# Optimization experiments

Hardware: AMD Instinct MI355X
Metric: run time of the kernel (lower is better)

The kernel has to match this reference:

```python
import jax, jax.numpy as jnp
import numpy as np
from jax import lax

NUM_VARS = 16384
NUM_CHECKS = 8192
BATCH = 32
MAX_ITER = 15
H_DENSITY = 0.001  # ~8 ones per column, LDPC-like Tanner graph


def setup_inputs() -> dict:
    key = jax.random.key(0)
    k_h, k_s, k_l = jax.random.split(key, 3)
    # Sparse binary parity-check matrix represented densely (same math).
    parity_matrix = (jax.random.uniform(k_h, (NUM_CHECKS, NUM_VARS)) < H_DENSITY).astype(jnp.float32)
    syndrome = jax.random.randint(k_s, (BATCH, NUM_CHECKS), 0, 2).astype(jnp.float32)
    channel_llrs = jax.random.normal(k_l, (BATCH, NUM_VARS), dtype=jnp.float32)
    w_vc = jnp.ones((1,), dtype=jnp.float32)
    w_cv = jnp.ones((1,), dtype=jnp.float32)
    damping = jnp.float32(0.5)
    return {
        "syndrome": syndrome,
        "parity_matrix": parity_matrix,
        "channel_llrs": channel_llrs,
        "w_vc": w_vc,
        "w_cv": w_cv,
        "damping": damping,
    }


def reference(syndrome, parity_matrix, channel_llrs, w_vc, w_cv, damping):
    # syndrome: (B, C); parity_matrix H: (C, V); channel_llrs: (B, V)
    s_sign = 1.0 - 2.0 * syndrome  # (B, C)

    def body(v_beliefs, _):
        # v -> c: sparse.mm(H, v^T)^T == v @ H^T  -> (B, C)
        v_to_c = w_vc * (v_beliefs @ parity_matrix.T)
        c_msg = s_sign * jnp.tanh(v_to_c * 0.5)  # (B, C)
        # c -> v: sparse.mm(H^T, c^T)^T == c @ H  -> (B, V)
        c_to_v = w_cv * (c_msg @ parity_matrix)
        v_new = damping * v_beliefs + (1.0 - damping) * (channel_llrs + c_to_v)
        return v_new, None

    v_beliefs, _ = lax.scan(body, channel_llrs, None, length=MAX_ITER)
    return jax.nn.sigmoid(-v_beliefs)  # (B, V) bit-flip probabilities
```

## Files before the change

### kernel.cpp

```cpp
#include <hip/hip_runtime.h>


#define C_NUM 8192
#define V_NUM 16384
#define B_NUM 32
#define RW 64
#define CW 32

__global__ void build_csr(const float* __restrict__ H,
                          int* __restrict__ row_cnt, int* __restrict__ col_cnt,
                          int* __restrict__ row_idx, int* __restrict__ col_idx) {
    const long long total4 = (long long)C_NUM * V_NUM / 4;
    const long long stride = (long long)gridDim.x * blockDim.x;
    for (long long t = (long long)blockIdx.x * blockDim.x + threadIdx.x;
         t < total4; t += stride) {
        float4 hv = ((const float4*)H)[t];
        long long e = t * 4;
        float vals[4] = {hv.x, hv.y, hv.z, hv.w};
#pragma unroll
        for (int k = 0; k < 4; ++k) {
            if (vals[k] != 0.0f) {
                long long ee = e + k;
                int c = (int)(ee >> 14);
                int v = (int)(ee & (V_NUM - 1));
                int rs = atomicAdd(&row_cnt[c], 1);
                if (rs < RW) row_idx[c * RW + rs] = v;
                int cs = atomicAdd(&col_cnt[v], 1);
                if (cs < CW) col_idx[v * CW + cs] = c;
            }
        }
    }
}

__global__ void init_state(const float* __restrict__ llr,
                           const float* __restrict__ synd,
                           float* __restrict__ beliefs, float* __restrict__ llr_t,
                           float* __restrict__ ssign_t) {
    int t = blockIdx.x * blockDim.x + threadIdx.x;
    if (t < V_NUM * B_NUM) {
        int b = t & (B_NUM - 1);
        int v = t >> 5;
        float x = llr[b * V_NUM + v];
        beliefs[t] = x;
        llr_t[t] = x;
    }
    if (t < C_NUM * B_NUM) {
        int b = t & (B_NUM - 1);
        int c = t >> 5;
        ssign_t[t] = 1.0f - 2.0f * synd[b * C_NUM + c];
    }
}

__global__ void vc_kernel(const float* __restrict__ beliefs,
                          const int* __restrict__ row_cnt,
                          const int* __restrict__ row_idx,
                          const float* __restrict__ ssign_t,
                          const float* __restrict__ w_vc_p,
                          float* __restrict__ cmsg) {
    int t = blockIdx.x * blockDim.x + threadIdx.x;
    if (t >= C_NUM * B_NUM) return;
    int b = t & (B_NUM - 1);
    int c = t >> 5;
    float w = w_vc_p[0];
    int n = row_cnt[c];
    if (n > RW) n = RW;
    const int* __restrict__ idx = &row_idx[c * RW];
    float sum = 0.0f;
    for (int j = 0; j < n; ++j)
        sum += beliefs[idx[j] * B_NUM + b];
    cmsg[t] = ssign_t[t] * tanhf(0.5f * w * sum);
}

__global__ void cv_kernel(const float* __restrict__ cmsg,
                          const int* __restrict__ col_cnt,
                          const int* __restrict__ col_idx,
                          const float* __restrict__ llr_t,
                          const float* __restrict__ beliefs_in,
                          float* __restrict__ beliefs_out,
                          const float* __restrict__ w_cv_p,
                          const float* __restrict__ damping_p) {
    int t = blockIdx.x * blockDim.x + threadIdx.x;
    if (t >= V_NUM * B_NUM) return;
    int b = t & (B_NUM - 1);
    int v = t >> 5;
    float w = w_cv_p[0];
    float d = damping_p[0];
    int n = col_cnt[v];
    if (n > CW) n = CW;
    const int* __restrict__ idx = &col_idx[v * CW];
    float sum = 0.0f;
    for (int j = 0; j < n; ++j)
        sum += cmsg[idx[j] * B_NUM + b];
    beliefs_out[t] = d * beliefs_in[t] + (1.0f - d) * (llr_t[t] + w * sum);
}

__global__ void final_kernel(const float* __restrict__ beliefs,
                             float* __restrict__ out) {
    int t = blockIdx.x * blockDim.x + threadIdx.x;
    if (t >= V_NUM * B_NUM) return;
    int v = t & (V_NUM - 1);
    int b = t >> 14;
    float x = beliefs[v * B_NUM + b];
    out[t] = 1.0f / (1.0f + __expf(x));
}

extern "C" void kernel_launch(void* const* d_in, const int* in_sizes, int n_in,
                              void* d_out, int out_size, void* d_ws, size_t ws_size,
                              hipStream_t stream) {
    const float* synd = (const float*)d_in[0];
    const float* H    = (const float*)d_in[1];
    const float* llr  = (const float*)d_in[2];
    const float* w_vc = (const float*)d_in[3];
    const float* w_cv = (const float*)d_in[4];
    const float* damp = (const float*)d_in[5];
    float* out = (float*)d_out;

    char* ws = (char*)d_ws;
    size_t off = 0;
    int* row_cnt = (int*)(ws + off); off += (size_t)C_NUM * 4;
    int* col_cnt = (int*)(ws + off); off += (size_t)V_NUM * 4;
    int* row_idx = (int*)(ws + off); off += (size_t)C_NUM * RW * 4;
    int* col_idx = (int*)(ws + off); off += (size_t)V_NUM * CW * 4;
    float* beliefs_a = (float*)(ws + off); off += (size_t)V_NUM * B_NUM * 4;
    float* beliefs_b = (float*)(ws + off); off += (size_t)V_NUM * B_NUM * 4;
    float* cmsg      = (float*)(ws + off); off += (size_t)C_NUM * B_NUM * 4;
    float* ssign_t   = (float*)(ws + off); off += (size_t)C_NUM * B_NUM * 4;
    float* llr_t     = (float*)(ws + off); off += (size_t)V_NUM * B_NUM * 4;

    hipMemsetAsync(row_cnt, 0, (size_t)(C_NUM + V_NUM) * 4, stream);

    build_csr<<<8192, 256, 0, stream>>>(H, row_cnt, col_cnt, row_idx, col_idx);
    init_state<<<(V_NUM * B_NUM + 255) / 256, 256, 0, stream>>>(
        llr, synd, beliefs_a, llr_t, ssign_t);

    float* cur = beliefs_a;
    float* nxt = beliefs_b;
    for (int it = 0; it < 15; ++it) {
        vc_kernel<<<(C_NUM * B_NUM + 255) / 256, 256, 0, stream>>>(
            cur, row_cnt, row_idx, ssign_t, w_vc, cmsg);
        cv_kernel<<<(V_NUM * B_NUM + 255) / 256, 256, 0, stream>>>(
            cmsg, col_cnt, col_idx, llr_t, cur, nxt, w_cv, damp);
        float* tmp = cur; cur = nxt; nxt = tmp;
    }
    final_kernel<<<(V_NUM * B_NUM + 255) / 256, 256, 0, stream>>>(cur, out);
}
```

Before: 1.094 ms.

## Fuse CSR build and all BP iterations into one cooperative persistent kernel

Replaces the memset, CSR build, init, 30 per-iteration kernels and the final kernel with a single cooperative kernel of 256 blocks of 1024 threads. Phases are separated by grid-wide barriers, and each thread owns fixed check and variable slots across iterations. The goal is to remove the per-launch overhead and the gaps between dependent kernels. In exchange, the grid-sync latency grows with this thread count, and streaming the large dense H matrix with a fixed, smaller resident grid may lower memory-level parallelism.

```diff
diff --git a/kernel.cpp b/kernel.cpp
--- a/kernel.cpp
+++ b/kernel.cpp
@@ -1,4 +1,7 @@
 #include <hip/hip_runtime.h>
+#include <hip/hip_cooperative_groups.h>
+
+namespace cg = cooperative_groups;
 
 
 #define C_NUM 8192
@@ -7,101 +10,111 @@
 #define RW 64
 #define CW 32
 
-__global__ void build_csr(const float* __restrict__ H,
-                          int* __restrict__ row_cnt, int* __restrict__ col_cnt,
-                          int* __restrict__ row_idx, int* __restrict__ col_idx) {
-    const long long total4 = (long long)C_NUM * V_NUM / 4;
-    const long long stride = (long long)gridDim.x * blockDim.x;
-    for (long long t = (long long)blockIdx.x * blockDim.x + threadIdx.x;
-         t < total4; t += stride) {
-        float4 hv = ((const float4*)H)[t];
-        long long e = t * 4;
-        float vals[4] = {hv.x, hv.y, hv.z, hv.w};
-#pragma unroll
-        for (int k = 0; k < 4; ++k) {
-            if (vals[k] != 0.0f) {
-                long long ee = e + k;
-                int c = (int)(ee >> 14);
-                int v = (int)(ee & (V_NUM - 1));
-                int rs = atomicAdd(&row_cnt[c], 1);
-                if (rs < RW) row_idx[c * RW + rs] = v;
-                int cs = atomicAdd(&col_cnt[v], 1);
-                if (cs < CW) col_idx[v * CW + cs] = c;
-            }
-        }
+#define GRID_BLOCKS 256
+#define BLOCK_THREADS 1024
+#define NTH (GRID_BLOCKS * BLOCK_THREADS)
+
+__global__ __launch_bounds__(BLOCK_THREADS, 4)
+void bp_fused(const float* __restrict__ H,
+              const float* __restrict__ synd,
+              const float* __restrict__ llr,
+              const float* __restrict__ w_vc_p,
+              const float* __restrict__ w_cv_p,
+              const float* __restrict__ damp_p,
+              int* __restrict__ row_cnt, int* __restrict__ col_cnt,
+              int* __restrict__ row_idx, int* __restrict__ col_idx,
+              float* __restrict__ beliefs_a, float* __restrict__ beliefs_b,
+              float* __restrict__ cmsg,
+              float* __restrict__ ssign_t, float* __restrict__ llr_t,
+              float* __restrict__ out) {
+    cg::grid_group grid = cg::this_grid();
+    const int tid = blockIdx.x * blockDim.x + threadIdx.x;
+
+    for (int i = tid; i < C_NUM + V_NUM; i += NTH) {
+        if (i < C_NUM) row_cnt[i] = 0;
+        else           col_cnt[i - C_NUM] = 0;
     }
-}
-
-__global__ void init_state(const float* __restrict__ llr,
-                           const float* __restrict__ synd,
-                           float* __restrict__ beliefs, float* __restrict__ llr_t,
-                           float* __restrict__ ssign_t) {
-    int t = blockIdx.x * blockDim.x + threadIdx.x;
-    if (t < V_NUM * B_NUM) {
+    for (int t = tid; t < V_NUM * B_NUM; t += NTH) {
         int b = t & (B_NUM - 1);
         int v = t >> 5;
         float x = llr[b * V_NUM + v];
-        beliefs[t] = x;
+        beliefs_a[t] = x;
         llr_t[t] = x;
     }
-    if (t < C_NUM * B_NUM) {
+    for (int t = tid; t < C_NUM * B_NUM; t += NTH) {
         int b = t & (B_NUM - 1);
         int c = t >> 5;
         ssign_t[t] = 1.0f - 2.0f * synd[b * C_NUM + c];
     }
-}
+    grid.sync();
 
-__global__ void vc_kernel(const float* __restrict__ beliefs,
-                          const int* __restrict__ row_cnt,
-                          const int* __restrict__ row_idx,
-                          const float* __restrict__ ssign_t,
-                          const float* __restrict__ w_vc_p,
-                          float* __restrict__ cmsg) {
-    int t = blockIdx.x * blockDim.x + threadIdx.x;
-    if (t >= C_NUM * B_NUM) return;
-    int b = t & (B_NUM - 1);
-    int c = t >> 5;
-    float w = w_vc_p[0];
-    int n = row_cnt[c];
-    if (n > RW) n = RW;
-    const int* __restrict__ idx = &row_idx[c * RW];
-    float sum = 0.0f;
-    for (int j = 0; j < n; ++j)
-        sum += beliefs[idx[j] * B_NUM + b];
-    cmsg[t] = ssign_t[t] * tanhf(0.5f * w * sum);
-}
+    {
+        const int total4 = C_NUM * V_NUM / 4;
+        for (int t = tid; t < total4; t += NTH) {
+            float4 hv = ((const float4*)H)[t];
+            int e = t * 4;
+            float vals[4] = {hv.x, hv.y, hv.z, hv.w};
+#pragma unroll
+            for (int k = 0; k < 4; ++k) {
+                if (vals[k] != 0.0f) {
+                    int ee = e + k;
+                    int c = ee >> 14;
+                    int v = ee & (V_NUM - 1);
+                    int rs = atomicAdd(&row_cnt[c], 1);
+                    if (rs < RW) row_idx[c * RW + rs] = v;
+                    int cs = atomicAdd(&col_cnt[v], 1);
+                    if (cs < CW) col_idx[v * CW + cs] = c;
+                }
+            }
+        }
+    }
+    grid.sync();
 
-__global__ void cv_kernel(const float* __restrict__ cmsg,
-                          const int* __restrict__ col_cnt,
-                          const int* __restrict__ col_idx,
-                          const float* __restrict__ llr_t,
-                          const float* __restrict__ beliefs_in,
-                          float* __restrict__ beliefs_out,
-                          const float* __restrict__ w_cv_p,
-                          const float* __restrict__ damping_p) {
-    int t = blockIdx.x * blockDim.x + threadIdx.x;
-    if (t >= V_NUM * B_NUM) return;
-    int b = t & (B_NUM - 1);
-    int v = t >> 5;
-    float w = w_cv_p[0];
-    float d = damping_p[0];
-    int n = col_cnt[v];
-    if (n > CW) n = CW;
-    const int* __restrict__ idx = &col_idx[v * CW];
-    float sum = 0.0f;
-    for (int j = 0; j < n; ++j)
-        sum += cmsg[idx[j] * B_NUM + b];
-    beliefs_out[t] = d * beliefs_in[t] + (1.0f - d) * (llr_t[t] + w * sum);
-}
+    const float w_vc = w_vc_p[0];
+    const float w_cv = w_cv_p[0];
+    const float d    = damp_p[0];
 
-__global__ void final_kernel(const float* __restrict__ beliefs,
-                             float* __restrict__ out) {
-    int t = blockIdx.x * blockDim.x + threadIdx.x;
-    if (t >= V_NUM * B_NUM) return;
-    int v = t & (V_NUM - 1);
-    int b = t >> 14;
-    float x = beliefs[v * B_NUM + b];
-    out[t] = 1.0f / (1.0f + __expf(x));
+    float* cur = beliefs_a;
+    float* nxt = beliefs_b;
+    for (int it = 0; it < 15; ++it) {
+        {
+            int t = tid;
+            int b = t & (B_NUM - 1);
+            int c = t >> 5;
+            int n = row_cnt[c];
+            if (n > RW) n = RW;
+            const int* __restrict__ idx = &row_idx[c * RW];
+            float sum = 0.0f;
+            for (int j = 0; j < n; ++j)
+                sum += cur[idx[j] * B_NUM + b];
+            cmsg[t] = ssign_t[t] * tanhf(0.5f * w_vc * sum);
+        }
+        grid.sync();
+#pragma unroll
+        for (int r = 0; r < 2; ++r) {
+            int t = tid + r * NTH;
+            int b = t & (B_NUM - 1);
+            int v = t >> 5;
+            int n = col_cnt[v];
+            if (n > CW) n = CW;
+            const int* __restrict__ idx = &col_idx[v * CW];
+            float sum = 0.0f;
+            for (int j = 0; j < n; ++j)
+                sum += cmsg[idx[j] * B_NUM + b];
+            nxt[t] = d * cur[t] + (1.0f - d) * (llr_t[t] + w_cv * sum);
+        }
+        grid.sync();
+        float* tmp = cur; cur = nxt; nxt = tmp;
+    }
+
+#pragma unroll
+    for (int r = 0; r < 2; ++r) {
+        int t = tid + r * NTH;
+        int v = t & (V_NUM - 1);
+        int b = t >> 14;
+        float x = cur[v * B_NUM + b];
+        out[t] = 1.0f / (1.0f + __expf(x));
+    }
 }
 
 extern "C" void kernel_launch(void* const* d_in, const int* in_sizes, int n_in,
@@ -127,20 +140,14 @@
     float* ssign_t   = (float*)(ws + off); off += (size_t)C_NUM * B_NUM * 4;
     float* llr_t     = (float*)(ws + off); off += (size_t)V_NUM * B_NUM * 4;
 
-    hipMemsetAsync(row_cnt, 0, (size_t)(C_NUM + V_NUM) * 4, stream);
-
-    build_csr<<<8192, 256, 0, stream>>>(H, row_cnt, col_cnt, row_idx, col_idx);
-    init_state<<<(V_NUM * B_NUM + 255) / 256, 256, 0, stream>>>(
-        llr, synd, beliefs_a, llr_t, ssign_t);
-
-    float* cur = beliefs_a;
-    float* nxt = beliefs_b;
-    for (int it = 0; it < 15; ++it) {
-        vc_kernel<<<(C_NUM * B_NUM + 255) / 256, 256, 0, stream>>>(
-            cur, row_cnt, row_idx, ssign_t, w_vc, cmsg);
-        cv_kernel<<<(V_NUM * B_NUM + 255) / 256, 256, 0, stream>>>(
-            cmsg, col_cnt, col_idx, llr_t, cur, nxt, w_cv, damp);
-        float* tmp = cur; cur = nxt; nxt = tmp;
-    }
-    final_kernel<<<(V_NUM * B_NUM + 255) / 256, 256, 0, stream>>>(cur, out);
+    void* args[] = {
+        (void*)&H, (void*)&synd, (void*)&llr,
+        (void*)&w_vc, (void*)&w_cv, (void*)&damp,
+        (void*)&row_cnt, (void*)&col_cnt, (void*)&row_idx, (void*)&col_idx,
+        (void*)&beliefs_a, (void*)&beliefs_b, (void*)&cmsg,
+        (void*)&ssign_t, (void*)&llr_t, (void*)&out
+    };
+    hipLaunchCooperativeKernel((const void*)bp_fused,
+                               dim3(GRID_BLOCKS), dim3(BLOCK_THREADS),
+                               args, 0, stream);
 }
```

Measured after the change: 2.040 ms. 1.86x slower.
